# Performance work log

Measured on AMD Instinct MI355X. Metric: run time of the kernel, lower is better.

Reference implementation:

```python
import jax, jax.numpy as jnp
import numpy as np

N_NODES = 50000
N_EDGES = 800000
IN_DIM = 256
HID = [256, 128]
NEG_SLOPE = 0.01  # F.leaky_relu default


def setup_inputs() -> dict:
    key = jax.random.key(0)
    ks = jax.random.split(key, 8)
    x = jax.random.normal(ks[0], (N_NODES, IN_DIM), dtype=jnp.float32)
    w1 = jax.random.normal(ks[1], (IN_DIM, HID[0]), dtype=jnp.float32) * (1.0 / np.sqrt(IN_DIM))
    b1 = jnp.zeros((HID[0],), dtype=jnp.float32)
    w2 = jax.random.normal(ks[2], (HID[0], HID[1]), dtype=jnp.float32) * (1.0 / np.sqrt(HID[0]))
    b2 = jnp.zeros((HID[1],), dtype=jnp.float32)
    src = jax.random.randint(ks[3], (N_EDGES,), 0, N_NODES, dtype=jnp.int32)
    dst = jax.random.randint(ks[4], (N_EDGES,), 0, N_NODES, dtype=jnp.int32)
    edge_weight = jax.random.uniform(ks[5], (N_EDGES,), dtype=jnp.float32)
    return {"x": x, "w1": w1, "b1": b1, "w2": w2, "b2": b2,
            "src": src, "dst": dst, "edge_weight": edge_weight}


def _gcn_layer(h, w, b, src, dst, ew, n_nodes):
    # GraphConvolution: support = h @ W ; out = spmm(adj, support) + b
    support = h @ w                              # [N, d_out]
    msg = support[src] * ew[:, None]             # [E, d_out] gather + scale
    agg = jax.ops.segment_sum(msg, dst, num_segments=n_nodes)  # [N, d_out]
    return agg + b


def reference(x, w1, b1, w2, b2, src, dst, edge_weight):
    # layer 1: GCN -> leaky_relu -> dropout(eval: identity)
    h = _gcn_layer(x, w1, b1, src, dst, edge_weight, N_NODES)
    h = jax.nn.leaky_relu(h, NEG_SLOPE)
    # layer 2
    h = _gcn_layer(h, w2, b2, src, dst, edge_weight, N_NODES)
    h = jax.nn.leaky_relu(h, NEG_SLOPE)
    return h
```

## Files before the change

kernel.cpp:

```cpp
#include <hip/hip_runtime.h>

#define NEG_SLOPE 0.01f

constexpr int N_NODES_C = 50000;
constexpr int N_EDGES_C = 800000;
constexpr int M_PAD = 50048;

typedef short bf16x8 __attribute__((ext_vector_type(8)));
typedef float f32x4 __attribute__((ext_vector_type(4)));

__device__ inline unsigned short f2bf(float f) {
  unsigned int u = __float_as_uint(f);
  u += 0x7FFF + ((u >> 16) & 1);
  return (unsigned short)(u >> 16);
}
__device__ inline float bf2f(unsigned int h16) {
  return __uint_as_float(h16 << 16);
}

constexpr int NB_CONVX = (M_PAD * 32) / 256;
constexpr int NB_W1 = (256 * 256) / 256;
constexpr int NB_W2 = (256 * 128) / 256;
constexpr int NB_HIST = N_EDGES_C / 256;
constexpr int NB_PRE = NB_CONVX + NB_W1 + NB_W2 + NB_HIST;

__global__ __launch_bounds__(256) void pre_kernel(
    const float* __restrict__ x, const float* __restrict__ w1,
    const float* __restrict__ w2, const int* __restrict__ dst,
    unsigned short* __restrict__ xb, unsigned short* __restrict__ w1T,
    unsigned short* __restrict__ w2T, int* __restrict__ counts) {
  const int bx = blockIdx.x;
  const int tid = threadIdx.x;
  if (bx < NB_CONVX) {
    int idx = bx * 256 + tid;
    int row = idx >> 5;
    int c8 = (idx & 31) << 3;
    uint4 v;
    if (row < N_NODES_C) {
      const float4* p = (const float4*)(x + (size_t)row * 256 + c8);
      float4 a = p[0], b = p[1];
      v.x = f2bf(a.x) | ((unsigned)f2bf(a.y) << 16);
      v.y = f2bf(a.z) | ((unsigned)f2bf(a.w) << 16);
      v.z = f2bf(b.x) | ((unsigned)f2bf(b.y) << 16);
      v.w = f2bf(b.z) | ((unsigned)f2bf(b.w) << 16);
    } else {
      v = make_uint4(0, 0, 0, 0);
    }
    *(uint4*)(xb + (size_t)row * 256 + c8) = v;
  } else if (bx < NB_CONVX + NB_W1) {
    int idx = (bx - NB_CONVX) * 256 + tid;
    int n = idx >> 8, k = idx & 255;
    w1T[idx] = f2bf(w1[(size_t)k * 256 + n]);
  } else if (bx < NB_CONVX + NB_W1 + NB_W2) {
    int idx = (bx - NB_CONVX - NB_W1) * 256 + tid;
    int n = idx >> 8, k = idx & 255;
    w2T[idx] = f2bf(w2[(size_t)k * 128 + n]);
  } else {
    int e = (bx - NB_CONVX - NB_W1 - NB_W2) * 256 + tid;
    atomicAdd(&counts[dst[e]], 1);
  }
}

constexpr int N_SCAN_BLKS = (N_NODES_C + 255) / 256;

__global__ __launch_bounds__(256) void scan_phase_a(const int* __restrict__ counts,
                                                    int* __restrict__ partial,
                                                    int* __restrict__ blk_sums) {
  __shared__ int s[256];
  const int t = threadIdx.x;
  const int i = blockIdx.x * 256 + t;
  const int v = (i < N_NODES_C) ? counts[i] : 0;
  s[t] = v;
  __syncthreads();
  for (int off = 1; off < 256; off <<= 1) {
    int u = (t >= off) ? s[t - off] : 0;
    __syncthreads();
    s[t] += u;
    __syncthreads();
  }
  if (i < N_NODES_C) partial[i] = s[t] - v;
  if (t == 255) blk_sums[blockIdx.x] = s[255];
}

__global__ __launch_bounds__(256) void scan_phase_b(const int* __restrict__ blk_sums,
                                                    int* __restrict__ blk_off) {
  __shared__ int s[256];
  const int t = threadIdx.x;
  const int v = (t < N_SCAN_BLKS) ? blk_sums[t] : 0;
  s[t] = v;
  __syncthreads();
  for (int off = 1; off < 256; off <<= 1) {
    int u = (t >= off) ? s[t - off] : 0;
    __syncthreads();
    s[t] += u;
    __syncthreads();
  }
  if (t < N_SCAN_BLKS) blk_off[t] = s[t] - v;
}

__global__ __launch_bounds__(256) void scan_phase_c(const int* __restrict__ partial,
                                                    const int* __restrict__ blk_off,
                                                    int* __restrict__ row_ptr,
                                                    int* __restrict__ cursor) {
  const int i = blockIdx.x * 256 + threadIdx.x;
  if (i < N_NODES_C) {
    const int r = partial[i] + blk_off[blockIdx.x];
    row_ptr[i] = r;
    cursor[i] = r;
  }
  if (i == 0) row_ptr[N_NODES_C] = N_EDGES_C;
}

__global__ __launch_bounds__(256) void fill_kernel(const int* __restrict__ src,
                                                   const int* __restrict__ dst,
                                                   const float* __restrict__ ew,
                                                   int* __restrict__ cursor,
                                                   uint2* __restrict__ s_meta) {
  int e = blockIdx.x * 256 + threadIdx.x;
  if (e < N_EDGES_C) {
    int p = atomicAdd(&cursor[dst[e]], 1);
    uint2 m;
    m.x = (unsigned)src[e];
    m.y = __float_as_uint(ew[e]);
    s_meta[p] = m;
  }
}


#define GLOAD_LDS16(g, l)                                              \
  __builtin_amdgcn_global_load_lds(                                    \
      (__attribute__((address_space(1))) void*)(g),                    \
      (__attribute__((address_space(3))) void*)(l), 16, 0, 0)

__global__ __launch_bounds__(256) void gemm_bf16_kernel(
    const unsigned short* __restrict__ A,
    const unsigned short* __restrict__ BT,
    unsigned short* __restrict__ C,
    int N) {
  constexpr int K = 256;
  __shared__ short Asm[128 * 32];
  __shared__ short Bsm[128 * 32];
  const int tid = threadIdx.x;
  const int lane = tid & 63, wave = tid >> 6;
  const int wm = wave & 1, wn = wave >> 1;
  const int row0 = blockIdx.y * 128, col0 = blockIdx.x * 128;

  const int ch0 = wave * 2, ch1 = wave * 2 + 1;
  const int o0 = ch0 * 512 + lane * 8;
  const int o1 = ch1 * 512 + lane * 8;
  const int r0 = o0 >> 5, c0 = o0 & 31;
  const int r1 = o1 >> 5, c1 = o1 & 31;

  f32x4 acc[4][4] = {};

  for (int k0 = 0; k0 < K; k0 += 32) {
    GLOAD_LDS16(A + (size_t)(row0 + r0) * K + k0 + c0, &Asm[ch0 * 512]);
    GLOAD_LDS16(A + (size_t)(row0 + r1) * K + k0 + c1, &Asm[ch1 * 512]);
    GLOAD_LDS16(BT + (size_t)(col0 + r0) * K + k0 + c0, &Bsm[ch0 * 512]);
    GLOAD_LDS16(BT + (size_t)(col0 + r1) * K + k0 + c1, &Bsm[ch1 * 512]);
    __builtin_amdgcn_s_waitcnt(0);
    __syncthreads();

    bf16x8 af[4], bf[4];
#pragma unroll
    for (int mt = 0; mt < 4; ++mt)
      af[mt] = *(const bf16x8*)&Asm[(wm * 64 + mt * 16 + (lane & 15)) * 32 + (lane >> 4) * 8];
#pragma unroll
    for (int nt = 0; nt < 4; ++nt)
      bf[nt] = *(const bf16x8*)&Bsm[(wn * 64 + nt * 16 + (lane & 15)) * 32 + (lane >> 4) * 8];
#pragma unroll
    for (int mt = 0; mt < 4; ++mt)
#pragma unroll
      for (int nt = 0; nt < 4; ++nt)
        acc[mt][nt] = __builtin_amdgcn_mfma_f32_16x16x32_bf16(af[mt], bf[nt], acc[mt][nt], 0, 0, 0);
    __syncthreads();
  }

  const int cl = lane & 15, rq = (lane >> 4) * 4;
#pragma unroll
  for (int mt = 0; mt < 4; ++mt) {
    const int rbase = row0 + wm * 64 + mt * 16 + rq;
#pragma unroll
    for (int nt = 0; nt < 4; ++nt) {
      const int col = col0 + wn * 64 + nt * 16 + cl;
      const size_t sbase = ((size_t)(col >> 5) * M_PAD) * 32 + (col & 31);
#pragma unroll
      for (int i = 0; i < 4; ++i)
        C[sbase + (size_t)(rbase + i) * 32] = f2bf(acc[mt][nt][i]);
    }
  }
}


__device__ inline void fma8(float* acc, uint4 v, float wt) {
  acc[0] += bf2f(v.x & 0xffffu) * wt;
  acc[1] += bf2f(v.x >> 16) * wt;
  acc[2] += bf2f(v.y & 0xffffu) * wt;
  acc[3] += bf2f(v.y >> 16) * wt;
  acc[4] += bf2f(v.z & 0xffffu) * wt;
  acc[5] += bf2f(v.z >> 16) * wt;
  acc[6] += bf2f(v.w & 0xffffu) * wt;
  acc[7] += bf2f(v.w >> 16) * wt;
}

template <int NSLICE, int OUT_D, bool OUT_BF16>
__global__ __launch_bounds__(256) void agg_quad_kernel(
    const unsigned short* __restrict__ supS,
    const uint2* __restrict__ s_meta, const int* __restrict__ row_ptr,
    const float* __restrict__ bias, unsigned short* __restrict__ out_bf,
    float* __restrict__ out_f, int n_total) {
  const int bx = blockIdx.x;
  const int slice = bx & (NSLICE - 1);
  const int group = bx / NSLICE;
  const int tid = threadIdx.x;
  const int quad = tid >> 2;
  const int dimg = tid & 3;
  const int n = group * 64 + quad;
  if (n >= n_total) return;
  const bool valid = n < N_NODES_C;
  const unsigned short* tab = supS + (size_t)slice * M_PAD * 32;

  float acc[8] = {};
  if (valid) {
    int j = row_ptr[n];
    const int end = row_ptr[n + 1];
    for (; j + 2 <= end; j += 2) {
      uint2 m0 = s_meta[j];
      uint2 m1 = s_meta[j + 1];
      uint4 v0 = *(const uint4*)(tab + m0.x * 32 + dimg * 8);
      uint4 v1 = *(const uint4*)(tab + m1.x * 32 + dimg * 8);
      fma8(acc, v0, __uint_as_float(m0.y));
      fma8(acc, v1, __uint_as_float(m1.y));
    }
    if (j < end) {
      uint2 m0 = s_meta[j];
      uint4 v0 = *(const uint4*)(tab + m0.x * 32 + dimg * 8);
      fma8(acc, v0, __uint_as_float(m0.y));
    }
  }

  const int dbase = slice * 32 + dimg * 8;
  if (OUT_BF16) {
    unsigned short o[8];
#pragma unroll
    for (int j = 0; j < 8; ++j) {
      float v = acc[j] + bias[dbase + j];
      v = v >= 0.f ? v : NEG_SLOPE * v;
      o[j] = f2bf(v);
    }
    uint4 pk;
    pk.x = o[0] | ((unsigned)o[1] << 16);
    pk.y = o[2] | ((unsigned)o[3] << 16);
    pk.z = o[4] | ((unsigned)o[5] << 16);
    pk.w = o[6] | ((unsigned)o[7] << 16);
    *(uint4*)(out_bf + (size_t)n * OUT_D + dbase) = pk;
  } else if (valid) {
    float r[8];
#pragma unroll
    for (int j = 0; j < 8; ++j) {
      float v = acc[j] + bias[dbase + j];
      r[j] = v >= 0.f ? v : NEG_SLOPE * v;
    }
    *(float4*)(out_f + (size_t)n * OUT_D + dbase) = make_float4(r[0], r[1], r[2], r[3]);
    *(float4*)(out_f + (size_t)n * OUT_D + dbase + 4) = make_float4(r[4], r[5], r[6], r[7]);
  }
}


extern "C" void kernel_launch(void* const* d_in, const int* in_sizes, int n_in,
                              void* d_out, int out_size, void* d_ws, size_t ws_size,
                              hipStream_t stream) {
  const float* x  = (const float*)d_in[0];
  const float* w1 = (const float*)d_in[1];
  const float* b1 = (const float*)d_in[2];
  const float* w2 = (const float*)d_in[3];
  const float* b2 = (const float*)d_in[4];
  const int*   src = (const int*)d_in[5];
  const int*   dst = (const int*)d_in[6];
  const float* ew  = (const float*)d_in[7];
  float* out = (float*)d_out;

  unsigned short* xb   = (unsigned short*)d_ws;
  unsigned short* a2b  = xb + (size_t)M_PAD * 256;
  unsigned short* sup1 = a2b + (size_t)M_PAD * 256;
  unsigned short* sup2 = sup1 + (size_t)M_PAD * 256;
  unsigned short* w1T  = sup2 + (size_t)M_PAD * 128;
  unsigned short* w2T  = w1T + 256 * 256;
  int* counts  = (int*)(w2T + 128 * 256);
  int* cursor  = counts + N_NODES_C;
  int* row_ptr = cursor + N_NODES_C;
  int* partial = row_ptr + (N_NODES_C + 1);
  int* blk_sums= partial + N_NODES_C;
  int* blk_off = blk_sums + 256;
  uint2* s_meta = (uint2*)(blk_off + 256 + 2);

  const int EB = (N_EDGES_C + 255) / 256;

  hipMemsetAsync(counts, 0, N_NODES_C * sizeof(int), stream);
  pre_kernel<<<NB_PRE, 256, 0, stream>>>(x, w1, w2, dst, xb, w1T, w2T, counts);

  scan_phase_a<<<N_SCAN_BLKS, 256, 0, stream>>>(counts, partial, blk_sums);
  scan_phase_b<<<1, 256, 0, stream>>>(blk_sums, blk_off);
  scan_phase_c<<<N_SCAN_BLKS, 256, 0, stream>>>(partial, blk_off, row_ptr, cursor);
  fill_kernel<<<EB, 256, 0, stream>>>(src, dst, ew, cursor, s_meta);

  gemm_bf16_kernel<<<dim3(2, M_PAD / 128), 256, 0, stream>>>(xb, w1T, sup1, 256);
  {
    const int groups = M_PAD / 64;
    agg_quad_kernel<8, 256, true><<<groups * 8, 256, 0, stream>>>(
        sup1, s_meta, row_ptr, b1, a2b, nullptr, M_PAD);
  }

  gemm_bf16_kernel<<<dim3(1, M_PAD / 128), 256, 0, stream>>>(a2b, w2T, sup2, 128);
  {
    const int groups = (N_NODES_C + 63) / 64;
    agg_quad_kernel<4, 128, false><<<groups * 4, 256, 0, stream>>>(
        sup2, s_meta, row_ptr, b2, nullptr, out, N_NODES_C);
  }
}
```

Baseline: 332.1 us.

## Pin aggregation feature slices to XCDs with persistent atomic work queues

The aggregation kernel becomes persistent. Each block reads its hardware XCC ID and picks the feature slice matching that die. Blocks then pull 64-node groups from a per-slice atomic counter until the work runs out. The aim is for each XCD's L2 to hold only one slice of the support table (about 3.2 MB for layer 1) instead of thrashing across all slices, with edge metadata streamed through non-temporal loads so it does not pollute the cache. The cost is a per-group atomic plus two barriers, and correctness depends on the launch placing blocks on every XCD so each slice gets processed.

After: 481.4 us. +44.9%, slower.

```diff
diff --git a/kernel.cpp b/kernel.cpp
--- a/kernel.cpp
+++ b/kernel.cpp
@@ -204,65 +204,74 @@
 }
 
 template <int NSLICE, int OUT_D, bool OUT_BF16>
-__global__ __launch_bounds__(256) void agg_quad_kernel(
+__global__ __launch_bounds__(256) void agg_xcd_kernel(
     const unsigned short* __restrict__ supS,
-    const uint2* __restrict__ s_meta, const int* __restrict__ row_ptr,
-    const float* __restrict__ bias, unsigned short* __restrict__ out_bf,
-    float* __restrict__ out_f, int n_total) {
-  const int bx = blockIdx.x;
-  const int slice = bx & (NSLICE - 1);
-  const int group = bx / NSLICE;
+    const unsigned long long* __restrict__ s_meta,
+    const int* __restrict__ row_ptr, const float* __restrict__ bias,
+    unsigned short* __restrict__ out_bf, float* __restrict__ out_f,
+    int* __restrict__ ctr, int n_groups) {
+  unsigned xcc;
+  asm volatile("s_getreg_b32 %0, hwreg(HW_REG_XCC_ID)" : "=s"(xcc));
+  const int slice = (int)(xcc & (NSLICE - 1));
+  const unsigned short* tab = supS + (size_t)slice * M_PAD * 32;
   const int tid = threadIdx.x;
   const int quad = tid >> 2;
   const int dimg = tid & 3;
-  const int n = group * 64 + quad;
-  if (n >= n_total) return;
-  const bool valid = n < N_NODES_C;
-  const unsigned short* tab = supS + (size_t)slice * M_PAD * 32;
-
-  float acc[8] = {};
-  if (valid) {
-    int j = row_ptr[n];
-    const int end = row_ptr[n + 1];
-    for (; j + 2 <= end; j += 2) {
-      uint2 m0 = s_meta[j];
-      uint2 m1 = s_meta[j + 1];
-      uint4 v0 = *(const uint4*)(tab + m0.x * 32 + dimg * 8);
-      uint4 v1 = *(const uint4*)(tab + m1.x * 32 + dimg * 8);
-      fma8(acc, v0, __uint_as_float(m0.y));
-      fma8(acc, v1, __uint_as_float(m1.y));
+  __shared__ int sh_group;
+
+  for (;;) {
+    if (tid == 0) sh_group = atomicAdd(&ctr[slice], 1);
+    __syncthreads();
+    const int group = sh_group;
+    __syncthreads();
+    if (group >= n_groups) break;
+
+    const int n = group * 64 + quad;
+    const bool valid = n < N_NODES_C;
+    float acc[8] = {};
+    if (valid) {
+      int j = row_ptr[n];
+      const int end = row_ptr[n + 1];
+      for (; j + 2 <= end; j += 2) {
+        unsigned long long m0 = __builtin_nontemporal_load(&s_meta[j]);
+        unsigned long long m1 = __builtin_nontemporal_load(&s_meta[j + 1]);
+        uint4 v0 = *(const uint4*)(tab + (unsigned)(m0 & 0xffffffffu) * 32 + dimg * 8);
+        uint4 v1 = *(const uint4*)(tab + (unsigned)(m1 & 0xffffffffu) * 32 + dimg * 8);
+        fma8(acc, v0, __uint_as_float((unsigned)(m0 >> 32)));
+        fma8(acc, v1, __uint_as_float((unsigned)(m1 >> 32)));
+      }
+      if (j < end) {
+        unsigned long long m0 = __builtin_nontemporal_load(&s_meta[j]);
+        uint4 v0 = *(const uint4*)(tab + (unsigned)(m0 & 0xffffffffu) * 32 + dimg * 8);
+        fma8(acc, v0, __uint_as_float((unsigned)(m0 >> 32)));
+      }
     }
-    if (j < end) {
-      uint2 m0 = s_meta[j];
-      uint4 v0 = *(const uint4*)(tab + m0.x * 32 + dimg * 8);
-      fma8(acc, v0, __uint_as_float(m0.y));
+
+    const int dbase = slice * 32 + dimg * 8;
+    if (OUT_BF16) {
+      unsigned short o[8];
+#pragma unroll
+      for (int j = 0; j < 8; ++j) {
+        float v = acc[j] + bias[dbase + j];
+        v = v >= 0.f ? v : NEG_SLOPE * v;
+        o[j] = f2bf(v);
+      }
+      uint4 pk;
+      pk.x = o[0] | ((unsigned)o[1] << 16);
+      pk.y = o[2] | ((unsigned)o[3] << 16);
+      pk.z = o[4] | ((unsigned)o[5] << 16);
+      pk.w = o[6] | ((unsigned)o[7] << 16);
+      *(uint4*)(out_bf + (size_t)n * OUT_D + dbase) = pk;
+    } else if (valid) {
+      float r[8];
+#pragma unroll
+      for (int j = 0; j < 8; ++j) {
+        float v = acc[j] + bias[dbase + j];
+        r[j] = v >= 0.f ? v : NEG_SLOPE * v;
+      }
+      *(float4*)(out_f + (size_t)n * OUT_D + dbase) = make_float4(r[0], r[1], r[2], r[3]);
+      *(float4*)(out_f + (size_t)n * OUT_D + dbase + 4) = make_float4(r[4], r[5], r[6], r[7]);
     }
-  }
-
-  const int dbase = slice * 32 + dimg * 8;
-  if (OUT_BF16) {
-    unsigned short o[8];
-#pragma unroll
-    for (int j = 0; j < 8; ++j) {
-      float v = acc[j] + bias[dbase + j];
-      v = v >= 0.f ? v : NEG_SLOPE * v;
-      o[j] = f2bf(v);
-    }
-    uint4 pk;
-    pk.x = o[0] | ((unsigned)o[1] << 16);
-    pk.y = o[2] | ((unsigned)o[3] << 16);
-    pk.z = o[4] | ((unsigned)o[5] << 16);
-    pk.w = o[6] | ((unsigned)o[7] << 16);
-    *(uint4*)(out_bf + (size_t)n * OUT_D + dbase) = pk;
-  } else if (valid) {
-    float r[8];
-#pragma unroll
-    for (int j = 0; j < 8; ++j) {
-      float v = acc[j] + bias[dbase + j];
-      r[j] = v >= 0.f ? v : NEG_SLOPE * v;
-    }
-    *(float4*)(out_f + (size_t)n * OUT_D + dbase) = make_float4(r[0], r[1], r[2], r[3]);
-    *(float4*)(out_f + (size_t)n * OUT_D + dbase + 4) = make_float4(r[4], r[5], r[6], r[7]);
   }
 }
 
@@ -292,11 +301,14 @@
   int* partial = row_ptr + (N_NODES_C + 1);
   int* blk_sums= partial + N_NODES_C;
   int* blk_off = blk_sums + 256;
-  uint2* s_meta = (uint2*)(blk_off + 256 + 2);
+  int* ctr1    = blk_off + 256;
+  int* ctr2    = ctr1 + 8;
+  uint2* s_meta = (uint2*)(ctr2 + 8);
 
   const int EB = (N_EDGES_C + 255) / 256;
 
   hipMemsetAsync(counts, 0, N_NODES_C * sizeof(int), stream);
+  hipMemsetAsync(ctr1, 0, 16 * sizeof(int), stream);
   pre_kernel<<<NB_PRE, 256, 0, stream>>>(x, w1, w2, dst, xb, w1T, w2T, counts);
 
   scan_phase_a<<<N_SCAN_BLKS, 256, 0, stream>>>(counts, partial, blk_sums);
@@ -304,17 +316,13 @@
   scan_phase_c<<<N_SCAN_BLKS, 256, 0, stream>>>(partial, blk_off, row_ptr, cursor);
   fill_kernel<<<EB, 256, 0, stream>>>(src, dst, ew, cursor, s_meta);
 
+  const int NGROUPS = M_PAD / 64;
+
   gemm_bf16_kernel<<<dim3(2, M_PAD / 128), 256, 0, stream>>>(xb, w1T, sup1, 256);
-  {
-    const int groups = M_PAD / 64;
-    agg_quad_kernel<8, 256, true><<<groups * 8, 256, 0, stream>>>(
-        sup1, s_meta, row_ptr, b1, a2b, nullptr, M_PAD);
-  }
+  agg_xcd_kernel<8, 256, true><<<2048, 256, 0, stream>>>(
+      sup1, (const unsigned long long*)s_meta, row_ptr, b1, a2b, nullptr, ctr1, NGROUPS);
 
   gemm_bf16_kernel<<<dim3(1, M_PAD / 128), 256, 0, stream>>>(a2b, w2T, sup2, 128);
-  {
-    const int groups = (N_NODES_C + 63) / 64;
-    agg_quad_kernel<4, 128, false><<<groups * 4, 256, 0, stream>>>(
-        sup2, s_meta, row_ptr, b2, nullptr, out, N_NODES_C);
-  }
-}
+  agg_xcd_kernel<4, 128, false><<<2048, 256, 0, stream>>>(
+      sup2, (const unsigned long long*)s_meta, row_ptr, b2, nullptr, out, ctr2, NGROUPS);
+}
```
